# Kernel tuning notes

Measured on AMD Instinct MI355X. Metric: run time of the kernel, lower is better.

Reference implementation:

```python
import jax, jax.numpy as jnp
import numpy as np

N = 10000          # nodes
E = 320000         # edges (avg degree 32)
IN_DIM = 128
H = 4              # num_head_NCLA
C = 64             # num_hidden (per-head out channels of conv1)
NEG_SLOPE = 0.2
BN_EPS = 1e-5


def setup_inputs() -> dict:
    key = jax.random.key(0)
    ks = jax.random.split(key, 8)
    x = jax.random.normal(ks[0], (N, IN_DIM), jnp.float32)
    edge_index = jax.random.randint(ks[1], (2, E), 0, N).astype(jnp.int64)
    # GATConv params: lin (no bias), att_src/att_dst [1,H,C], final bias [H*C]
    W = jax.random.normal(ks[2], (IN_DIM, H * C), jnp.float32) / np.sqrt(IN_DIM).astype(np.float32)
    att_src = jax.random.normal(ks[3], (H, C), jnp.float32) * 0.1
    att_dst = jax.random.normal(ks[4], (H, C), jnp.float32) * 0.1
    bias = jnp.zeros((H * C,), jnp.float32)
    # bn1 affine params (shared across both BN applications, as in source)
    gamma = jnp.ones((H * C,), jnp.float32)
    beta = jnp.zeros((H * C,), jnp.float32)
    return dict(x=x, edge_index=edge_index, W=W, att_src=att_src,
                att_dst=att_dst, bias=bias, gamma=gamma, beta=beta)


def _batchnorm(x, gamma, beta):
    # BatchNorm1d, training-mode stats (batch mean, biased variance)
    mu = jnp.mean(x, axis=0)
    var = jnp.mean(jnp.square(x - mu), axis=0)
    return (x - mu) * jax.lax.rsqrt(var + BN_EPS) * gamma + beta


def _gat_conv(x, edge_index, W, att_src, att_dst, bias):
    src, dst = edge_index[0], edge_index[1]
    xp = (x @ W).reshape(-1, H, C)                      # [N,H,C]
    a_src = jnp.einsum('nhc,hc->nh', xp, att_src)       # [N,H]
    a_dst = jnp.einsum('nhc,hc->nh', xp, att_dst)       # [N,H]
    logits = a_src[src] + a_dst[dst]                    # [E,H]
    logits = jnp.where(logits >= 0, logits, NEG_SLOPE * logits)  # leaky_relu
    # scatter-softmax over incoming edges of each dst node
    m = jax.ops.segment_max(logits, dst, num_segments=N)         # [N,H]
    m = jnp.where(jnp.isfinite(m), m, 0.0)              # empty segments -> 0
    e = jnp.exp(logits - m[dst])                        # [E,H]
    denom = jax.ops.segment_sum(e, dst, num_segments=N)          # [N,H]
    alpha = e / (denom[dst] + 1e-16)                    # [E,H]
    msg = xp[src] * alpha[:, :, None]                   # [E,H,C]
    out = jax.ops.segment_sum(msg, dst, num_segments=N) # [N,H,C]
    return out.reshape(-1, H * C) + bias, alpha


def reference(x, edge_index, W, att_src, att_dst, bias, gamma, beta):
    x1, alpha = _gat_conv(x, edge_index, W, att_src, att_dst, bias)
    x2 = _batchnorm(x1, gamma, beta)
    x_ = _batchnorm(jax.nn.elu(x2), gamma, beta)        # bn1 reused, as in source
    heads = jnp.moveaxis(x_.reshape(-1, H, C), 1, 0)    # [H,N,C]: per-head splits
    return heads, alpha
```

## Files before the change

### kernel.cpp

```cpp
#include <hip/hip_runtime.h>
#include <math.h>

#define INDIM 128
#define HC 256
#define NH 4
#define CAP 128
#define NSHARD 64
#define BROWS 20

typedef unsigned short ushort_t;

__device__ __forceinline__ unsigned int f2bf_u(float f) {
  unsigned int u = __float_as_uint(f);
  return (u + 0x7FFFu + ((u >> 16) & 1u)) >> 16;
}
__device__ __forceinline__ float bf2f(ushort_t u) {
  return __uint_as_float(((unsigned int)u) << 16);
}

__global__ __launch_bounds__(256) void gemm_att_bucket_kernel(
    const float* __restrict__ x, const float* __restrict__ W,
    const float* __restrict__ att_s, const float* __restrict__ att_d,
    const int* __restrict__ dst, int* __restrict__ cnt,
    int* __restrict__ bucket, int E, int epb, ushort_t* __restrict__ xpb,
    float* __restrict__ a_src, float* __restrict__ a_dst, int N) {
  constexpr int RM = 16;
  __shared__ __align__(16) float xs[RM * INDIM];
  __shared__ __align__(16) float4 wq[32 * 64];
  int tid = threadIdx.x;
  int n0 = blockIdx.x * RM;
  int nrows = min(RM, N - n0);

  if (nrows > 0) {
    if (nrows == RM) {
      const float4* xg = (const float4*)(x + (size_t)n0 * INDIM);
      float4* xs4 = (float4*)xs;
      xs4[tid] = xg[tid];
      xs4[tid + 256] = xg[tid + 256];
    } else {
      for (int i = tid; i < RM * INDIM; i += 256) {
        int r = i / INDIM;
        xs[i] = (r < nrows) ? x[(size_t)(n0 + r) * INDIM + (i % INDIM)] : 0.f;
      }
    }

    int lane = tid & 63;
    int wv = tid >> 6;
    int row0 = wv * 4;

    float4 acc[4];
#pragma unroll
    for (int r = 0; r < 4; ++r) acc[r] = make_float4(0.f, 0.f, 0.f, 0.f);

    const float4* W4 = (const float4*)W;
#pragma unroll 1
    for (int p = 0; p < 4; ++p) {
      if (p) __syncthreads();
      const float4* Wg = W4 + (size_t)p * 2048;
#pragma unroll
      for (int j = 0; j < 8; ++j) wq[tid + j * 256] = Wg[tid + j * 256];
      __syncthreads();
#pragma unroll 1
      for (int c = 0; c < 4; ++c) {
        int kl = c * 8;
        int kg = p * 32 + kl;
        float4 w[8];
#pragma unroll
        for (int j = 0; j < 8; ++j) w[j] = wq[(kl + j) * 64 + lane];
#pragma unroll
        for (int r = 0; r < 4; ++r) {
          float4 xa = *(const float4*)&xs[(row0 + r) * INDIM + kg];
          float4 xb = *(const float4*)&xs[(row0 + r) * INDIM + kg + 4];
          acc[r].x = fmaf(xb.w, w[7].x, fmaf(xb.z, w[6].x, fmaf(xb.y, w[5].x, fmaf(xb.x, w[4].x,
                     fmaf(xa.w, w[3].x, fmaf(xa.z, w[2].x, fmaf(xa.y, w[1].x, fmaf(xa.x, w[0].x, acc[r].x))))))));
          acc[r].y = fmaf(xb.w, w[7].y, fmaf(xb.z, w[6].y, fmaf(xb.y, w[5].y, fmaf(xb.x, w[4].y,
                     fmaf(xa.w, w[3].y, fmaf(xa.z, w[2].y, fmaf(xa.y, w[1].y, fmaf(xa.x, w[0].y, acc[r].y))))))));
          acc[r].z = fmaf(xb.w, w[7].z, fmaf(xb.z, w[6].z, fmaf(xb.y, w[5].z, fmaf(xb.x, w[4].z,
                     fmaf(xa.w, w[3].z, fmaf(xa.z, w[2].z, fmaf(xa.y, w[1].z, fmaf(xa.x, w[0].z, acc[r].z))))))));
          acc[r].w = fmaf(xb.w, w[7].w, fmaf(xb.z, w[6].w, fmaf(xb.y, w[5].w, fmaf(xb.x, w[4].w,
                     fmaf(xa.w, w[3].w, fmaf(xa.z, w[2].w, fmaf(xa.y, w[1].w, fmaf(xa.x, w[0].w, acc[r].w))))))));
        }
      }
    }

    int col = lane * 4;
    float4 as4 = *(const float4*)&att_s[col];
    float4 ad4 = *(const float4*)&att_d[col];
    int h = lane >> 4;
#pragma unroll
    for (int r = 0; r < 4; ++r) {
      int row = row0 + r;
      if (row >= nrows) break;
      float4 a = acc[r];
      uint2 pk;
      pk.x = f2bf_u(a.x) | (f2bf_u(a.y) << 16);
      pk.y = f2bf_u(a.z) | (f2bf_u(a.w) << 16);
      *(uint2*)&xpb[(size_t)(n0 + row) * HC + col] = pk;
      float ps = a.x * as4.x + a.y * as4.y + a.z * as4.z + a.w * as4.w;
      float pd = a.x * ad4.x + a.y * ad4.y + a.z * ad4.z + a.w * ad4.w;
#pragma unroll
      for (int o = 8; o > 0; o >>= 1) {
        ps += __shfl_xor(ps, o);
        pd += __shfl_xor(pd, o);
      }
      if ((lane & 15) == 0) {
        a_src[(n0 + row) * NH + h] = ps;
        a_dst[(n0 + row) * NH + h] = pd;
      }
    }
  }

  int e0 = blockIdx.x * epb;
  int e1 = min(e0 + epb, E);
  for (int e = e0 + tid; e < e1; e += 256) {
    int d = dst[e];
    int pos = atomicAdd(&cnt[d], 1);
    if (pos < CAP) bucket[(size_t)d * CAP + pos] = e;
  }
}

__global__ __launch_bounds__(256) void node_kernel(
    const int* __restrict__ cnt, const int* __restrict__ bucket,
    const int* __restrict__ src_arr, const float* __restrict__ a_src,
    const float* __restrict__ a_dst, const ushort_t* __restrict__ xpb,
    const float* __restrict__ bias, float* __restrict__ x1,
    float* __restrict__ alpha_out, float* __restrict__ shards, int N) {
  int n = blockIdx.x;
  int tid = threadIdx.x;
  int lane = tid & 63, wv = tid >> 6;
  int deg = min(cnt[n], CAP);
  float bv = bias[tid];
  int shb = (n & (NSHARD - 1)) * (2 * HC);
  if (deg == 0) {
    x1[(size_t)n * HC + tid] = bv;
    atomicAdd(&shards[shb + tid], bv);
    atomicAdd(&shards[shb + HC + tid], bv * bv);
    return;
  }
  const int* brow = bucket + (size_t)n * CAP;

  __shared__ float m_s[NH], d_s[NH];
  __shared__ __align__(16) float alpha_lds[NH * CAP];
  __shared__ __align__(16) int src_lds[CAP];

  {
    int h = wv;
    float adst = a_dst[n * NH + h];
    float m = -INFINITY, s = 0.f;
    for (int i = lane; i < deg; i += 64) {
      int sidx = src_arr[brow[i]];
      if (h == 0) src_lds[i] = sidx;
      float l = a_src[sidx * NH + h] + adst;
      l = (l >= 0.f) ? l : 0.2f * l;
      if (l > m) { s = s * __expf(m - l) + 1.f; m = l; }
      else s += __expf(l - m);
    }
#pragma unroll
    for (int o = 32; o > 0; o >>= 1) {
      float m2 = __shfl_xor(m, o);
      float s2 = __shfl_xor(s, o);
      float M = fmaxf(m, m2);
      float sa = (m > -INFINITY) ? s * __expf(m - M) : 0.f;
      float sb = (m2 > -INFINITY) ? s2 * __expf(m2 - M) : 0.f;
      m = M; s = sa + sb;
    }
    if (lane == 0) { m_s[h] = m; d_s[h] = s + 1e-16f; }
  }
  __syncthreads();

  float m_r[NH], dinv_r[NH], adst_r[NH];
#pragma unroll
  for (int h = 0; h < NH; ++h) {
    m_r[h] = m_s[h];
    dinv_r[h] = 1.0f / d_s[h];
    adst_r[h] = a_dst[n * NH + h];
  }

  int cpad = (deg + 3) & ~3;
  if (tid < deg) {
    int sidx = src_lds[tid];
    float4 as4 = *(const float4*)&a_src[sidx * NH];
    const float* ap = (const float*)&as4;
    float4 av;
    float* avp = (float*)&av;
#pragma unroll
    for (int h = 0; h < NH; ++h) {
      float l = ap[h] + adst_r[h];
      l = (l >= 0.f) ? l : 0.2f * l;
      float a = __expf(l - m_r[h]) * dinv_r[h];
      alpha_lds[h * CAP + tid] = a;
      avp[h] = a;
    }
    *(float4*)&alpha_out[(size_t)brow[tid] * NH] = av;
  } else if (tid < cpad) {
    src_lds[tid] = 0;
#pragma unroll
    for (int h = 0; h < NH; ++h) alpha_lds[h * CAP + tid] = 0.f;
  }
  __syncthreads();

  float acc0 = 0.f, acc1 = 0.f, acc2 = 0.f, acc3 = 0.f;
  int hbase = wv * CAP;
  for (int i = 0; i < cpad; i += 4) {
    float4 a4 = *(const float4*)&alpha_lds[hbase + i];
    int4 s4 = *(const int4*)&src_lds[i];
    ushort_t u0 = xpb[(size_t)s4.x * HC + tid];
    ushort_t u1 = xpb[(size_t)s4.y * HC + tid];
    ushort_t u2 = xpb[(size_t)s4.z * HC + tid];
    ushort_t u3 = xpb[(size_t)s4.w * HC + tid];
    acc0 = fmaf(a4.x, bf2f(u0), acc0);
    acc1 = fmaf(a4.y, bf2f(u1), acc1);
    acc2 = fmaf(a4.z, bf2f(u2), acc2);
    acc3 = fmaf(a4.w, bf2f(u3), acc3);
  }
  float v = (acc0 + acc1) + (acc2 + acc3) + bv;
  x1[(size_t)n * HC + tid] = v;
  atomicAdd(&shards[shb + tid], v);
  atomicAdd(&shards[shb + HC + tid], v * v);
}

__global__ __launch_bounds__(256) void bn_stats2_kernel(
    const float* __restrict__ x1, const float* __restrict__ shards,
    const float* __restrict__ gamma, const float* __restrict__ beta,
    float* __restrict__ sums2, int N) {
  int t = threadIdx.x;
  float s1 = 0.f, q1 = 0.f;
#pragma unroll
  for (int k = 0; k < NSHARD; ++k) {
    s1 += shards[k * (2 * HC) + t];
    q1 += shards[k * (2 * HC) + HC + t];
  }
  float mu = s1 * (1.f / N);
  float var = q1 * (1.f / N) - mu * mu;
  float inv = rsqrtf(var + 1e-5f);
  float g = gamma[t], b = beta[t];
  int r0 = blockIdx.x * BROWS;
  int rend = min(r0 + BROWS, N);
  float s = 0.f, q = 0.f;
  for (int r = r0; r < rend; ++r) {
    float v = x1[(size_t)r * HC + t];
    float x2 = fmaf((v - mu) * inv, g, b);
    float e = x2 > 0.f ? x2 : expm1f(x2);
    s += e; q = fmaf(e, e, q);
  }
  atomicAdd(&sums2[t], s);
  atomicAdd(&sums2[HC + t], q);
}

__global__ __launch_bounds__(256) void bn_final_kernel(
    const float* __restrict__ x1, const float* __restrict__ shards,
    const float* __restrict__ sums2, const float* __restrict__ gamma,
    const float* __restrict__ beta, float* __restrict__ out, int N) {
  int t = threadIdx.x;
  float s1 = 0.f, q1 = 0.f;
#pragma unroll
  for (int k = 0; k < NSHARD; ++k) {
    s1 += shards[k * (2 * HC) + t];
    q1 += shards[k * (2 * HC) + HC + t];
  }
  float mu1 = s1 * (1.f / N);
  float var1 = q1 * (1.f / N) - mu1 * mu1;
  float inv1 = rsqrtf(var1 + 1e-5f);
  float mu2 = sums2[t] * (1.f / N);
  float var2 = sums2[HC + t] * (1.f / N) - mu2 * mu2;
  float inv2 = rsqrtf(var2 + 1e-5f);
  float g = gamma[t], b = beta[t];
  int h = t >> 6, c = t & 63;
  int r0 = blockIdx.x * BROWS;
  int rend = min(r0 + BROWS, N);
  for (int r = r0; r < rend; ++r) {
    float v = x1[(size_t)r * HC + t];
    float x2 = fmaf((v - mu1) * inv1, g, b);
    float e = x2 > 0.f ? x2 : expm1f(x2);
    out[(size_t)h * N * 64 + (size_t)r * 64 + c] = fmaf((e - mu2) * inv2, g, b);
  }
}

extern "C" void kernel_launch(void* const* d_in, const int* in_sizes, int n_in,
                              void* d_out, int out_size, void* d_ws, size_t ws_size,
                              hipStream_t stream) {
  const float* x     = (const float*)d_in[0];
  const int*   edge  = (const int*)d_in[1];
  const float* W     = (const float*)d_in[2];
  const float* att_s = (const float*)d_in[3];
  const float* att_d = (const float*)d_in[4];
  const float* bias  = (const float*)d_in[5];
  const float* gamma = (const float*)d_in[6];
  const float* beta  = (const float*)d_in[7];

  int N = in_sizes[0] / INDIM;
  int E = in_sizes[1] / 2;
  const int* src = edge;
  const int* dst = edge + E;

  char* ws = (char*)d_ws;
  size_t o = 0;
  auto alloc = [&](size_t bytes) {
    void* p = ws + o;
    o += (bytes + 255) & ~(size_t)255;
    return p;
  };
  ushort_t* xpb     = (ushort_t*)alloc((size_t)N * HC * 2);
  float* x1         = (float*)alloc((size_t)N * HC * 4);
  float* a_src      = (float*)alloc((size_t)N * NH * 4);
  float* a_dst      = (float*)alloc((size_t)N * NH * 4);
  char*  zbase      = (char*)alloc(0);
  int*   cnt        = (int*)alloc((size_t)N * 4);
  float* shards     = (float*)alloc((size_t)NSHARD * 2 * HC * 4);
  float* sums2      = (float*)alloc(2 * HC * 4);
  size_t zbytes     = (size_t)((char*)alloc(0) - zbase);
  int*   bucket     = (int*)alloc((size_t)N * CAP * 4);

  float* out_heads = (float*)d_out;
  float* out_alpha = out_heads + (size_t)NH * N * 64;

  hipMemsetAsync(zbase, 0, zbytes, stream);

  int gblocks = (N + 15) / 16;
  int epb = (E + gblocks - 1) / gblocks;
  gemm_att_bucket_kernel<<<gblocks, 256, 0, stream>>>(
      x, W, att_s, att_d, dst, cnt, bucket, E, epb, xpb, a_src, a_dst, N);
  node_kernel<<<N, 256, 0, stream>>>(cnt, bucket, src, a_src, a_dst, xpb, bias,
                                     x1, out_alpha, shards, N);
  int bnb = (N + BROWS - 1) / BROWS;
  bn_stats2_kernel<<<bnb, 256, 0, stream>>>(x1, shards, gamma, beta, sums2, N);
  bn_final_kernel<<<bnb, 256, 0, stream>>>(x1, shards, sums2, gamma, beta,
                                           out_heads, N);
}
```

Baseline: 105.1 us.

## Process one destination node per wavefront instead of per block

The node kernel now assigns each of the four wavefronts in a block its own destination node, replacing the block-per-node layout and its two __syncthreads barriers. Each lane handles all four heads for its edges during the online softmax and caches logits, source and edge ids in per-wave LDS. In aggregation each lane gathers four contiguous bf16 channels with a single 8-byte load. This removes block-wide synchronisation and per-node launch granularity, and widens memory accesses. In exchange each lane does four times the softmax work and per-lane atomics become scalar per channel.

```diff
diff --git a/kernel.cpp b/kernel.cpp
--- a/kernel.cpp
+++ b/kernel.cpp
@@ -125,98 +125,127 @@
     const float* __restrict__ a_dst, const ushort_t* __restrict__ xpb,
     const float* __restrict__ bias, float* __restrict__ x1,
     float* __restrict__ alpha_out, float* __restrict__ shards, int N) {
-  int n = blockIdx.x;
   int tid = threadIdx.x;
   int lane = tid & 63, wv = tid >> 6;
+  int n = blockIdx.x * 4 + wv;
+  if (n >= N) return;
+
+  __shared__ __align__(16) float l_sm[4][NH * CAP];
+  __shared__ __align__(16) int si_sm[4][CAP];
+  __shared__ __align__(16) int ei_sm[4][CAP];
+  float* s_l = l_sm[wv];
+  int* s_idx = si_sm[wv];
+  int* s_eid = ei_sm[wv];
+
+  int c0 = lane * 4;
+  float4 bv = *(const float4*)&bias[c0];
   int deg = min(cnt[n], CAP);
-  float bv = bias[tid];
   int shb = (n & (NSHARD - 1)) * (2 * HC);
   if (deg == 0) {
-    x1[(size_t)n * HC + tid] = bv;
-    atomicAdd(&shards[shb + tid], bv);
-    atomicAdd(&shards[shb + HC + tid], bv * bv);
+    *(float4*)&x1[(size_t)n * HC + c0] = bv;
+    atomicAdd(&shards[shb + c0 + 0], bv.x);
+    atomicAdd(&shards[shb + c0 + 1], bv.y);
+    atomicAdd(&shards[shb + c0 + 2], bv.z);
+    atomicAdd(&shards[shb + c0 + 3], bv.w);
+    atomicAdd(&shards[shb + HC + c0 + 0], bv.x * bv.x);
+    atomicAdd(&shards[shb + HC + c0 + 1], bv.y * bv.y);
+    atomicAdd(&shards[shb + HC + c0 + 2], bv.z * bv.z);
+    atomicAdd(&shards[shb + HC + c0 + 3], bv.w * bv.w);
     return;
   }
   const int* brow = bucket + (size_t)n * CAP;
-
-  __shared__ float m_s[NH], d_s[NH];
-  __shared__ __align__(16) float alpha_lds[NH * CAP];
-  __shared__ __align__(16) int src_lds[CAP];
-
-  {
-    int h = wv;
-    float adst = a_dst[n * NH + h];
-    float m = -INFINITY, s = 0.f;
-    for (int i = lane; i < deg; i += 64) {
-      int sidx = src_arr[brow[i]];
-      if (h == 0) src_lds[i] = sidx;
-      float l = a_src[sidx * NH + h] + adst;
-      l = (l >= 0.f) ? l : 0.2f * l;
-      if (l > m) { s = s * __expf(m - l) + 1.f; m = l; }
-      else s += __expf(l - m);
-    }
-#pragma unroll
-    for (int o = 32; o > 0; o >>= 1) {
-      float m2 = __shfl_xor(m, o);
-      float s2 = __shfl_xor(s, o);
-      float M = fmaxf(m, m2);
-      float sa = (m > -INFINITY) ? s * __expf(m - M) : 0.f;
-      float sb = (m2 > -INFINITY) ? s2 * __expf(m2 - M) : 0.f;
-      m = M; s = sa + sb;
-    }
-    if (lane == 0) { m_s[h] = m; d_s[h] = s + 1e-16f; }
-  }
-  __syncthreads();
-
-  float m_r[NH], dinv_r[NH], adst_r[NH];
-#pragma unroll
-  for (int h = 0; h < NH; ++h) {
-    m_r[h] = m_s[h];
-    dinv_r[h] = 1.0f / d_s[h];
-    adst_r[h] = a_dst[n * NH + h];
-  }
-
+  float4 ad4 = *(const float4*)&a_dst[(size_t)n * NH];
+
+  float mx = -INFINITY, my = -INFINITY, mz = -INFINITY, mw = -INFINITY;
+  float sx = 0.f, sy = 0.f, sz = 0.f, sw = 0.f;
+  for (int i = lane; i < deg; i += 64) {
+    int e = brow[i];
+    int sidx = src_arr[e];
+    s_eid[i] = e;
+    s_idx[i] = sidx;
+    float4 l4 = *(const float4*)&a_src[(size_t)sidx * NH];
+    l4.x += ad4.x; l4.y += ad4.y; l4.z += ad4.z; l4.w += ad4.w;
+    l4.x = l4.x >= 0.f ? l4.x : 0.2f * l4.x;
+    l4.y = l4.y >= 0.f ? l4.y : 0.2f * l4.y;
+    l4.z = l4.z >= 0.f ? l4.z : 0.2f * l4.z;
+    l4.w = l4.w >= 0.f ? l4.w : 0.2f * l4.w;
+    s_l[0 * CAP + i] = l4.x;
+    s_l[1 * CAP + i] = l4.y;
+    s_l[2 * CAP + i] = l4.z;
+    s_l[3 * CAP + i] = l4.w;
+    if (l4.x > mx) { sx = sx * __expf(mx - l4.x) + 1.f; mx = l4.x; } else sx += __expf(l4.x - mx);
+    if (l4.y > my) { sy = sy * __expf(my - l4.y) + 1.f; my = l4.y; } else sy += __expf(l4.y - my);
+    if (l4.z > mz) { sz = sz * __expf(mz - l4.z) + 1.f; mz = l4.z; } else sz += __expf(l4.z - mz);
+    if (l4.w > mw) { sw = sw * __expf(mw - l4.w) + 1.f; mw = l4.w; } else sw += __expf(l4.w - mw);
+  }
   int cpad = (deg + 3) & ~3;
-  if (tid < deg) {
-    int sidx = src_lds[tid];
-    float4 as4 = *(const float4*)&a_src[sidx * NH];
-    const float* ap = (const float*)&as4;
-    float4 av;
-    float* avp = (float*)&av;
-#pragma unroll
-    for (int h = 0; h < NH; ++h) {
-      float l = ap[h] + adst_r[h];
-      l = (l >= 0.f) ? l : 0.2f * l;
-      float a = __expf(l - m_r[h]) * dinv_r[h];
-      alpha_lds[h * CAP + tid] = a;
-      avp[h] = a;
-    }
-    *(float4*)&alpha_out[(size_t)brow[tid] * NH] = av;
-  } else if (tid < cpad) {
-    src_lds[tid] = 0;
-#pragma unroll
-    for (int h = 0; h < NH; ++h) alpha_lds[h * CAP + tid] = 0.f;
-  }
-  __syncthreads();
-
-  float acc0 = 0.f, acc1 = 0.f, acc2 = 0.f, acc3 = 0.f;
-  int hbase = wv * CAP;
+  for (int i = deg + lane; i < cpad; i += 64) {
+    s_idx[i] = 0;
+    s_l[0 * CAP + i] = 0.f;
+    s_l[1 * CAP + i] = 0.f;
+    s_l[2 * CAP + i] = 0.f;
+    s_l[3 * CAP + i] = 0.f;
+  }
+#pragma unroll
+  for (int o = 32; o > 0; o >>= 1) {
+    float m2, s2, M;
+    m2 = __shfl_xor(mx, o); s2 = __shfl_xor(sx, o); M = fmaxf(mx, m2);
+    sx = ((mx > -INFINITY) ? sx * __expf(mx - M) : 0.f) + ((m2 > -INFINITY) ? s2 * __expf(m2 - M) : 0.f);
+    mx = M;
+    m2 = __shfl_xor(my, o); s2 = __shfl_xor(sy, o); M = fmaxf(my, m2);
+    sy = ((my > -INFINITY) ? sy * __expf(my - M) : 0.f) + ((m2 > -INFINITY) ? s2 * __expf(m2 - M) : 0.f);
+    my = M;
+    m2 = __shfl_xor(mz, o); s2 = __shfl_xor(sz, o); M = fmaxf(mz, m2);
+    sz = ((mz > -INFINITY) ? sz * __expf(mz - M) : 0.f) + ((m2 > -INFINITY) ? s2 * __expf(m2 - M) : 0.f);
+    mz = M;
+    m2 = __shfl_xor(mw, o); s2 = __shfl_xor(sw, o); M = fmaxf(mw, m2);
+    sw = ((mw > -INFINITY) ? sw * __expf(mw - M) : 0.f) + ((m2 > -INFINITY) ? s2 * __expf(m2 - M) : 0.f);
+    mw = M;
+  }
+  float dix = 1.f / (sx + 1e-16f);
+  float diy = 1.f / (sy + 1e-16f);
+  float diz = 1.f / (sz + 1e-16f);
+  float diw = 1.f / (sw + 1e-16f);
+
+  for (int i = lane; i < deg; i += 64) {
+    float4 a4;
+    a4.x = __expf(s_l[0 * CAP + i] - mx) * dix;
+    a4.y = __expf(s_l[1 * CAP + i] - my) * diy;
+    a4.z = __expf(s_l[2 * CAP + i] - mz) * diz;
+    a4.w = __expf(s_l[3 * CAP + i] - mw) * diw;
+    s_l[0 * CAP + i] = a4.x;
+    s_l[1 * CAP + i] = a4.y;
+    s_l[2 * CAP + i] = a4.z;
+    s_l[3 * CAP + i] = a4.w;
+    *(float4*)&alpha_out[(size_t)s_eid[i] * NH] = a4;
+  }
+
+  int h = lane >> 4;
+  const float* ah = &s_l[h * CAP];
+  float ax = 0.f, ay = 0.f, az = 0.f, aw = 0.f;
   for (int i = 0; i < cpad; i += 4) {
-    float4 a4 = *(const float4*)&alpha_lds[hbase + i];
-    int4 s4 = *(const int4*)&src_lds[i];
-    ushort_t u0 = xpb[(size_t)s4.x * HC + tid];
-    ushort_t u1 = xpb[(size_t)s4.y * HC + tid];
-    ushort_t u2 = xpb[(size_t)s4.z * HC + tid];
-    ushort_t u3 = xpb[(size_t)s4.w * HC + tid];
-    acc0 = fmaf(a4.x, bf2f(u0), acc0);
-    acc1 = fmaf(a4.y, bf2f(u1), acc1);
-    acc2 = fmaf(a4.z, bf2f(u2), acc2);
-    acc3 = fmaf(a4.w, bf2f(u3), acc3);
-  }
-  float v = (acc0 + acc1) + (acc2 + acc3) + bv;
-  x1[(size_t)n * HC + tid] = v;
-  atomicAdd(&shards[shb + tid], v);
-  atomicAdd(&shards[shb + HC + tid], v * v);
+    float a0 = ah[i], a1 = ah[i + 1], a2 = ah[i + 2], a3 = ah[i + 3];
+    int i0 = s_idx[i], i1 = s_idx[i + 1], i2 = s_idx[i + 2], i3 = s_idx[i + 3];
+    uint2 p0 = *(const uint2*)&xpb[(size_t)i0 * HC + c0];
+    uint2 p1 = *(const uint2*)&xpb[(size_t)i1 * HC + c0];
+    uint2 p2 = *(const uint2*)&xpb[(size_t)i2 * HC + c0];
+    uint2 p3 = *(const uint2*)&xpb[(size_t)i3 * HC + c0];
+    ax = fmaf(a3, bf2f((ushort_t)p3.x), fmaf(a2, bf2f((ushort_t)p2.x), fmaf(a1, bf2f((ushort_t)p1.x), fmaf(a0, bf2f((ushort_t)p0.x), ax))));
+    ay = fmaf(a3, bf2f((ushort_t)(p3.x >> 16)), fmaf(a2, bf2f((ushort_t)(p2.x >> 16)), fmaf(a1, bf2f((ushort_t)(p1.x >> 16)), fmaf(a0, bf2f((ushort_t)(p0.x >> 16)), ay))));
+    az = fmaf(a3, bf2f((ushort_t)p3.y), fmaf(a2, bf2f((ushort_t)p2.y), fmaf(a1, bf2f((ushort_t)p1.y), fmaf(a0, bf2f((ushort_t)p0.y), az))));
+    aw = fmaf(a3, bf2f((ushort_t)(p3.y >> 16)), fmaf(a2, bf2f((ushort_t)(p2.y >> 16)), fmaf(a1, bf2f((ushort_t)(p1.y >> 16)), fmaf(a0, bf2f((ushort_t)(p0.y >> 16)), aw))));
+  }
+  float4 v;
+  v.x = ax + bv.x; v.y = ay + bv.y; v.z = az + bv.z; v.w = aw + bv.w;
+  *(float4*)&x1[(size_t)n * HC + c0] = v;
+  atomicAdd(&shards[shb + c0 + 0], v.x);
+  atomicAdd(&shards[shb + c0 + 1], v.y);
+  atomicAdd(&shards[shb + c0 + 2], v.z);
+  atomicAdd(&shards[shb + c0 + 3], v.w);
+  atomicAdd(&shards[shb + HC + c0 + 0], v.x * v.x);
+  atomicAdd(&shards[shb + HC + c0 + 1], v.y * v.y);
+  atomicAdd(&shards[shb + HC + c0 + 2], v.z * v.z);
+  atomicAdd(&shards[shb + HC + c0 + 3], v.w * v.w);
 }
 
 __global__ __launch_bounds__(256) void bn_stats2_kernel(
@@ -320,8 +349,8 @@
   int epb = (E + gblocks - 1) / gblocks;
   gemm_att_bucket_kernel<<<gblocks, 256, 0, stream>>>(
       x, W, att_s, att_d, dst, cnt, bucket, E, epb, xpb, a_src, a_dst, N);
-  node_kernel<<<N, 256, 0, stream>>>(cnt, bucket, src, a_src, a_dst, xpb, bias,
-                                     x1, out_alpha, shards, N);
+  node_kernel<<<(N + 3) / 4, 256, 0, stream>>>(cnt, bucket, src, a_src, a_dst,
+                                               xpb, bias, x1, out_alpha, shards, N);
   int bnb = (N + BROWS - 1) / BROWS;
   bn_stats2_kernel<<<bnb, 256, 0, stream>>>(x1, shards, gamma, beta, sums2, N);
   bn_final_kernel<<<bnb, 256, 0, stream>>>(x1, shards, sums2, gamma, beta,
```

Measured after the change: 163.6 us. +55.6%, slower.
